# Kernel tuning notes

Measured on AMD Instinct MI355X. Metric: run time of the kernel, lower is better.

The kernel has to match this reference:

```python
import jax, jax.numpy as jnp
import numpy as np

B, T, C, H = 2, 4096, 512, 8
D = C // H          # head_size = 64
FF = 4 * C          # 2048
EPS = 1e-5


def _layernorm(x, g, b):
    mu = jnp.mean(x, axis=-1, keepdims=True)
    var = jnp.mean(jnp.square(x - mu), axis=-1, keepdims=True)
    return (x - mu) * jax.lax.rsqrt(var + EPS) * g + b


def setup_inputs() -> dict:
    key = jax.random.key(0)
    ks = jax.random.split(key, 10)
    s = 0.02
    return {
        "x":  jax.random.normal(ks[0], (B, T, C), dtype=jnp.float32),
        # per-head K/Q/V linears (bias=False) packed as [C, C] = concat over heads
        "Wq": jax.random.normal(ks[1], (C, C), dtype=jnp.float32) * s,
        "Wk": jax.random.normal(ks[2], (C, C), dtype=jnp.float32) * s,
        "Wv": jax.random.normal(ks[3], (C, C), dtype=jnp.float32) * s,
        "Wo": jax.random.normal(ks[4], (C, C), dtype=jnp.float32) * s,
        "bo": jnp.zeros((C,), dtype=jnp.float32),
        "W1": jax.random.normal(ks[5], (C, FF), dtype=jnp.float32) * s,
        "b1": jnp.zeros((FF,), dtype=jnp.float32),
        "W2": jax.random.normal(ks[6], (FF, C), dtype=jnp.float32) * s,
        "b2": jnp.zeros((C,), dtype=jnp.float32),
        "g1": jnp.ones((C,), dtype=jnp.float32),
        "be1": jnp.zeros((C,), dtype=jnp.float32),
        "g2": jnp.ones((C,), dtype=jnp.float32),
        "be2": jnp.zeros((C,), dtype=jnp.float32),
    }


def reference(x, Wq, Wk, Wv, Wo, bo, W1, b1, W2, b2, g1, be1, g2, be2):
    # --- self-attention on ln1(x), residual add ---
    h = _layernorm(x, g1, be1)                              # [B,T,C]
    q = (h @ Wq).reshape(B, T, H, D)
    k = (h @ Wk).reshape(B, T, H, D)
    v = (h @ Wv).reshape(B, T, H, D)
    # NOTE: original scales by C**-0.5 (n_embd), NOT head_size**-0.5
    scores = jnp.einsum("bthd,bshd->bhts", q, k) * (C ** -0.5)  # [B,H,T,T]
    causal = jnp.tril(jnp.ones((T, T), dtype=bool))
    scores = jnp.where(causal, scores, -jnp.inf)
    wei = jax.nn.softmax(scores, axis=-1)                   # dropout = identity (eval)
    attn = jnp.einsum("bhts,bshd->bthd", wei, v).reshape(B, T, C)
    x = x + (attn @ Wo + bo)                                # proj dropout = identity
    # --- feed-forward on ln2(x), residual add ---
    h2 = _layernorm(x, g2, be2)
    ff = jax.nn.relu(h2 @ W1 + b1) @ W2 + b2                # dropout = identity
    return x + ff
```

## Files before the change

kernel.cpp:

```cpp
#include <hip/hip_runtime.h>

typedef __attribute__((ext_vector_type(8))) __bf16 bf16x8;
typedef __attribute__((ext_vector_type(4))) __bf16 bf16x4;
typedef __attribute__((ext_vector_type(4))) float f32x4;
typedef __attribute__((ext_vector_type(4))) unsigned int u32x4;
typedef __attribute__((ext_vector_type(4))) unsigned short u16x4;
typedef __attribute__((ext_vector_type(8))) unsigned short u16x8;
typedef __attribute__((ext_vector_type(4))) short s16x4;
typedef unsigned short u16;

static __device__ __forceinline__ u16 f2b(float f) {
    unsigned u = __builtin_bit_cast(unsigned, f);
    u = (u + 0x7FFFu + ((u >> 16) & 1u)) >> 16;
    return (u16)u;
}
static __device__ __forceinline__ float b2f(u16 u) {
    return __builtin_bit_cast(float, ((unsigned)u) << 16);
}
static __device__ __forceinline__ float fexp2(float x) {
#if __has_builtin(__builtin_amdgcn_exp2f)
    return __builtin_amdgcn_exp2f(x);
#else
    return exp2f(x);
#endif
}
static __device__ __forceinline__ f32x4 mfma16(bf16x4 a, bf16x4 b, f32x4 c) {
#if __has_builtin(__builtin_amdgcn_mfma_f32_16x16x16_bf16)
    return __builtin_amdgcn_mfma_f32_16x16x16_bf16(a, b, c, 0, 0, 0);
#else
    return __builtin_amdgcn_mfma_f32_16x16x16bf16_1k(
        __builtin_bit_cast(s16x4, a), __builtin_bit_cast(s16x4, b), c, 0, 0, 0);
#endif
}

static __device__ __forceinline__ void gload16(const u16* g, u16* l) {
    __builtin_amdgcn_global_load_lds(
        (const __attribute__((address_space(1))) unsigned int*)g,
        (__attribute__((address_space(3))) unsigned int*)l, 16, 0, 0);
}

__global__ __launch_bounds__(256) void prep_w(
    const float* __restrict__ Wq, const float* __restrict__ Wk,
    const float* __restrict__ Wv, const float* __restrict__ Wo,
    const float* __restrict__ W1, const float* __restrict__ W2,
    u16* __restrict__ WqkvT, u16* __restrict__ WoT,
    u16* __restrict__ W1T, u16* __restrict__ W2T)
{
    const int z = blockIdx.z;
    const float* src; u16* dst; int K, N;
    if (z == 0)      { src = Wq; dst = WqkvT;             K = 512;  N = 512;  }
    else if (z == 1) { src = Wk; dst = WqkvT + 512*512;   K = 512;  N = 512;  }
    else if (z == 2) { src = Wv; dst = WqkvT + 1024*512;  K = 512;  N = 512;  }
    else if (z == 3) { src = Wo; dst = WoT;               K = 512;  N = 512;  }
    else if (z == 4) { src = W1; dst = W1T;               K = 512;  N = 2048; }
    else             { src = W2; dst = W2T;               K = 2048; N = 512;  }
    const int nt = blockIdx.x * 32, kt = blockIdx.y * 32;
    if (nt >= N || kt >= K) return;
    __shared__ float tile[32][33];
    const int tx = threadIdx.x & 31, ty = threadIdx.x >> 5;
    #pragma unroll
    for (int i = 0; i < 4; ++i)
        tile[ty + i*8][tx] = src[(size_t)(kt + ty + i*8) * N + nt + tx];
    __syncthreads();
    #pragma unroll
    for (int i = 0; i < 4; ++i)
        dst[(size_t)(nt + ty + i*8) * K + kt + tx] = f2b(tile[tx][ty + i*8]);
}

__global__ __launch_bounds__(256) void ln_rows(
    const float* __restrict__ x, const float* __restrict__ g,
    const float* __restrict__ b, u16* __restrict__ out)
{
    const int row = blockIdx.x * 4 + (threadIdx.x >> 6);
    const int lane = threadIdx.x & 63;
    const float* xr = x + (size_t)row * 512;
    f32x4 v0 = *(const f32x4*)(xr + lane * 4);
    f32x4 v1 = *(const f32x4*)(xr + 256 + lane * 4);
    float s = v0[0]+v0[1]+v0[2]+v0[3]+v1[0]+v1[1]+v1[2]+v1[3];
    #pragma unroll
    for (int o = 1; o < 64; o <<= 1) s += __shfl_xor(s, o);
    const float mu = s * (1.0f / 512.0f);
    float s2 = 0.f;
    #pragma unroll
    for (int i = 0; i < 4; ++i) { float d0 = v0[i]-mu, d1 = v1[i]-mu; s2 += d0*d0 + d1*d1; }
    #pragma unroll
    for (int o = 1; o < 64; o <<= 1) s2 += __shfl_xor(s2, o);
    const float inv = rsqrtf(s2 * (1.0f/512.0f) + 1e-5f);
    f32x4 g0 = *(const f32x4*)(g + lane*4), g1 = *(const f32x4*)(g + 256 + lane*4);
    f32x4 b0 = *(const f32x4*)(b + lane*4), b1 = *(const f32x4*)(b + 256 + lane*4);
    u16x4 p0, p1;
    #pragma unroll
    for (int i = 0; i < 4; ++i) {
        p0[i] = f2b((v0[i]-mu)*inv*g0[i] + b0[i]);
        p1[i] = f2b((v1[i]-mu)*inv*g1[i] + b1[i]);
    }
    u16* orow = out + (size_t)row * 512;
    *(u16x4*)(orow + lane*4)       = p0;
    *(u16x4*)(orow + 256 + lane*4) = p1;
}

template<int FLAGS>
__global__ __launch_bounds__(256) void gemm_bt(
    const u16* __restrict__ A, const u16* __restrict__ BT,
    const int N, const int K,
    const float* __restrict__ bias, const float* __restrict__ res,
    void* __restrict__ outv, u16* __restrict__ vt)
{
    __shared__ __attribute__((aligned(16))) u16 As[3][4096];
    __shared__ __attribute__((aligned(16))) u16 Bs[3][4096];
    const int tid = threadIdx.x, lane = tid & 63, w = tid >> 6;
    const int wr2 = w >> 1, wc = w & 1;
    const int m0 = blockIdx.y << 7, n0 = blockIdx.x << 7;
    const int g = lane >> 4, c = lane & 15;
    const f32x4 fz = {0.f, 0.f, 0.f, 0.f};

    f32x4 acc[4][4];
    #pragma unroll
    for (int m = 0; m < 4; ++m)
      #pragma unroll
      for (int n = 0; n < 4; ++n) acc[m][n] = fz;

    const int srow = tid >> 2;
    const int scs = (((tid & 3) ^ (srow & 3)) * 8);
    const u16* Ag = A  + (size_t)(m0 + srow)*K + scs;
    const u16* Bg = BT + (size_t)(n0 + srow)*K + scs;
    const size_t rstep = (size_t)64 * K;

    const int nkt = K >> 5;
    auto stage = [&](int slot, int kt) {
        const int k0 = kt << 5;
        u16* ad = &As[0][0] + slot*4096 + w*512;
        u16* bd = &Bs[0][0] + slot*4096 + w*512;
        gload16(Ag + k0,         ad); gload16(Ag + rstep + k0, ad + 2048);
        gload16(Bg + k0,         bd); gload16(Bg + rstep + k0, bd + 2048);
    };
    stage(0, 0);
    stage(1, (1 < nkt) ? 1 : 0);

    int rd = 0, wrs = 2;
    for (int kt = 0; kt < nkt; ++kt) {
        asm volatile("s_waitcnt vmcnt(4)" ::: "memory");
        __builtin_amdgcn_s_barrier();
        asm volatile("" ::: "memory");
        stage(wrs, (kt + 2 < nkt) ? (kt + 2) : (nkt - 1));
        const u16* Ab = &As[0][0] + rd*4096;
        const u16* Bb = &Bs[0][0] + rd*4096;
        bf16x8 af[4], bfr[4];
        #pragma unroll
        for (int m = 0; m < 4; ++m) {
            const int row = wr2*64 + m*16 + c;
            af[m] = *(const bf16x8*)(Ab + row*32 + (((g*16) ^ ((row&3)<<4)) >> 1));
        }
        #pragma unroll
        for (int n = 0; n < 4; ++n) {
            const int row = wc*64 + n*16 + c;
            bfr[n] = *(const bf16x8*)(Bb + row*32 + (((g*16) ^ ((row&3)<<4)) >> 1));
        }
        #pragma unroll
        for (int m = 0; m < 4; ++m)
          #pragma unroll
          for (int n = 0; n < 4; ++n)
            acc[m][n] = __builtin_amdgcn_mfma_f32_16x16x32_bf16(af[m], bfr[n], acc[m][n], 0, 0, 0);
        rd = (rd == 2) ? 0 : rd + 1;
        wrs = (wrs == 2) ? 0 : wrs + 1;
    }

    #pragma unroll
    for (int m = 0; m < 4; ++m) {
        const int row = m0 + wr2*64 + m*16 + 4*g;
        #pragma unroll
        for (int n = 0; n < 4; ++n) {
            const int col = n0 + wc*64 + n*16 + c;
            const float bv = (FLAGS & 1) ? bias[col] : 0.0f;
            float vv[4];
            #pragma unroll
            for (int r = 0; r < 4; ++r) {
                float v = acc[m][n][r] + bv;
                if (FLAGS & 16) v *= (col < 512) ? 0.0637587246f : 1.0f;
                if (FLAGS & 2) v += res[(size_t)(row + r)*N + col];
                if (FLAGS & 4) v = fmaxf(v, 0.0f);
                vv[r] = v;
            }
            if ((FLAGS & 32) && col >= 1024) {
                u16x4 pv;
                #pragma unroll
                for (int r = 0; r < 4; ++r) pv[r] = f2b(vv[r]);
                *(u16x4*)(vt + (size_t)((row >> 12)*512 + (col - 1024))*4096
                             + (row & 4095)) = pv;
            } else if (FLAGS & 8) {
                #pragma unroll
                for (int r = 0; r < 4; ++r)
                    ((float*)outv)[(size_t)(row + r)*N + col] = vv[r];
            } else {
                #pragma unroll
                for (int r = 0; r < 4; ++r)
                    ((u16*)outv)[(size_t)(row + r)*N + col] = f2b(vv[r]);
            }
        }
    }
}

__global__ __launch_bounds__(256, 3) void attn_fwd(
    const u16* __restrict__ qkv, const u16* __restrict__ vT,
    u16* __restrict__ part, u16* __restrict__ att)
{
    const int bh = blockIdx.y, b = bh >> 3, h = bh & 7;
    const int i = blockIdx.x;
    int qt, t0, t1, single;
    if (i < 32) { qt = i; t0 = 0; t1 = qt + 1; single = 1; }
    else {
        const int j = i - 32; qt = 32 + (j >> 1);
        const int nt = qt + 1, tm = nt >> 1;
        t0 = (j & 1) ? tm : 0; t1 = (j & 1) ? nt : tm; single = 0;
    }

    const int tid = threadIdx.x, lane = tid & 63, w = tid >> 6;
    const int g = lane >> 4, c16 = lane & 15;
    __shared__ __attribute__((aligned(16))) u16 smem[24576 + 512];
    u16* Wb = smem + w*6144;
    float* lbuf = (float*)(smem + 24576);

    const u16* qp  = qkv + (size_t)b*4096*1536 + h*64;
    const u16* kp  = qp + 512;
    const u16* vtp = vT + (size_t)bh*64*4096;

    const u16* kgA = kp + (size_t)(16*w + (lane>>3))*1536
                        + (((lane&7) ^ ((lane>>3)&7)) * 8);
    const u16* kgB = kgA + (size_t)8*1536;
    const int sd = lane >> 1;
    const u16* vgA = vtp + (size_t)sd*4096 + 16*w + (((lane&1) ^ ((sd>>2)&1)) * 8);
    const u16* vgB = vgA + (size_t)32*4096;

    const int kOff0 = c16*64 + ((g ^ (c16&7)) * 8);
    const int kOff1 = c16*64 + (((4+g) ^ (c16&7)) * 8);
    const int vroff = c16*16 + (((g>>1) ^ ((c16>>2)&1)) * 8) + (g&1)*4;

    const int Q0 = qt*64;
    bf16x8 qB[4][2];
    #pragma unroll
    for (int sub = 0; sub < 4; ++sub) {
        const u16* qr = qp + (size_t)(Q0 + sub*16 + c16)*1536 + g*8;
        qB[sub][0] = *(const bf16x8*)(qr);
        qB[sub][1] = *(const bf16x8*)(qr + 32);
    }

    const f32x4 fz = {0.f,0.f,0.f,0.f};
    f32x4 oacc[4][4];
    #pragma unroll
    for (int dt = 0; dt < 4; ++dt)
      #pragma unroll
      for (int sub = 0; sub < 4; ++sub) oacc[dt][sub] = fz;
    float lsum[4] = {0.f, 0.f, 0.f, 0.f};

    {
        const int tp1 = (t0+1 < t1) ? (t0+1) : (t1-1);
        u16* s0 = Wb + (t0 % 3)*2048;
        const size_t ko0 = (size_t)(t0 << 6)*1536; const int kv0 = t0 << 6;
        gload16(kgA + ko0, s0);        gload16(kgB + ko0, s0 + 512);
        gload16(vgA + kv0, s0 + 1024); gload16(vgB + kv0, s0 + 1536);
        u16* s1 = Wb + (tp1 % 3)*2048;
        const size_t ko1 = (size_t)(tp1 << 6)*1536; const int kv1 = tp1 << 6;
        gload16(kgA + ko1, s1);        gload16(kgB + ko1, s1 + 512);
        gload16(vgA + kv1, s1 + 1024); gload16(vgB + kv1, s1 + 1536);
    }
    int rd = t0 % 3;
    int wrs = rd + 2; if (wrs >= 3) wrs -= 3;

    for (int t = t0; t < t1; ++t) {
        asm volatile("s_waitcnt vmcnt(4)" ::: "memory");
        const u16* slotR = Wb + rd*2048;
        const bf16x8 kc0 = *(const bf16x8*)(slotR + kOff0);
        const bf16x8 kc1 = *(const bf16x8*)(slotR + kOff1);
        bf16x4 va[4];
        #pragma unroll
        for (int dt = 0; dt < 4; ++dt)
            va[dt] = *(const bf16x4*)(slotR + 1024 + dt*256 + vroff);
        {
            const int tp = (t+2 < t1) ? (t+2) : (t1-1);
            u16* slotW = Wb + wrs*2048;
            const size_t ko = (size_t)(tp << 6)*1536; const int kv = tp << 6;
            gload16(kgA + ko, slotW);        gload16(kgB + ko, slotW + 512);
            gload16(vgA + kv, slotW + 1024); gload16(vgB + kv, slotW + 1536);
        }
        f32x4 s[4];
        #pragma unroll
        for (int sub = 0; sub < 4; ++sub) {
            f32x4 sv = __builtin_amdgcn_mfma_f32_16x16x32_bf16(kc0, qB[sub][0], fz, 0, 0, 0);
            s[sub]   = __builtin_amdgcn_mfma_f32_16x16x32_bf16(kc1, qB[sub][1], sv, 0, 0, 0);
        }
        bf16x4 pt[4];
        if (t < qt) {
            #pragma unroll
            for (int sub = 0; sub < 4; ++sub) {
                float p0 = fexp2(s[sub][0]), p1 = fexp2(s[sub][1]);
                float p2 = fexp2(s[sub][2]), p3 = fexp2(s[sub][3]);
                lsum[sub] += (p0 + p1) + (p2 + p3);
                bf16x4 pv;
                pv[0] = (__bf16)p0; pv[1] = (__bf16)p1;
                pv[2] = (__bf16)p2; pv[3] = (__bf16)p3;
                pt[sub] = pv;
            }
        } else {
            const int kvbase = t*64 + 16*w + 4*g;
            #pragma unroll
            for (int sub = 0; sub < 4; ++sub) {
                const int qi = Q0 + sub*16 + c16;
                bf16x4 pv; float a = 0.f;
                #pragma unroll
                for (int r = 0; r < 4; ++r) {
                    float p = (kvbase + r <= qi) ? fexp2(s[sub][r]) : 0.0f;
                    a += p; pv[r] = (__bf16)p;
                }
                lsum[sub] += a; pt[sub] = pv;
            }
        }
        #pragma unroll
        for (int dt = 0; dt < 4; ++dt)
          #pragma unroll
          for (int sub = 0; sub < 4; ++sub)
            oacc[dt][sub] = mfma16(va[dt], pt[sub], oacc[dt][sub]);
        rd  = (rd  == 2) ? 0 : rd  + 1;
        wrs = (wrs == 2) ? 0 : wrs + 1;
    }

    #pragma unroll
    for (int sub = 0; sub < 4; ++sub) {
        float v = lsum[sub];
        v += __shfl_xor(v, 16);
        v += __shfl_xor(v, 32);
        if (g == 0) lbuf[w*64 + sub*16 + c16] = v;
    }
    __syncthreads();
    float ltot[4];
    #pragma unroll
    for (int sub = 0; sub < 4; ++sub) {
        const int qr = sub*16 + c16;
        ltot[sub] = lbuf[qr] + lbuf[64 + qr] + lbuf[128 + qr] + lbuf[192 + qr];
    }

    float* img = (float*)smem;
    f32x4 ofin[4];
    const int roff = (g ^ (c16 & 3))*4;
    #pragma unroll
    for (int dt = 0; dt < 4; ++dt) {
        #pragma unroll
        for (int sub = 0; sub < 4; ++sub)
            *(f32x4*)(img + w*1024 + (sub*16 + c16)*16 + roff) = oacc[dt][sub];
        __syncthreads();
        if (w == dt) {
            #pragma unroll
            for (int sub = 0; sub < 4; ++sub) {
                const int off = (sub*16 + c16)*16 + roff;
                f32x4 a0 = *(const f32x4*)(img + off);
                f32x4 a1 = *(const f32x4*)(img + 1024 + off);
                f32x4 a2 = *(const f32x4*)(img + 2048 + off);
                f32x4 a3 = *(const f32x4*)(img + 3072 + off);
                ofin[sub] = (a0 + a1) + (a2 + a3);
            }
        }
        __syncthreads();
    }

    const int dbase = 16*w + 4*g;
    if (single) {
        #pragma unroll
        for (int sub = 0; sub < 4; ++sub) {
            const int qrow = sub*16 + c16;
            const float inv = 1.0f / ltot[sub];
            const f32x4 o = ofin[sub];
            u16x4 ov;
            ov[0] = f2b(o[0]*inv); ov[1] = f2b(o[1]*inv);
            ov[2] = f2b(o[2]*inv); ov[3] = f2b(o[3]*inv);
            *(u16x4*)(att + (size_t)(b*4096 + Q0 + qrow)*512 + h*64 + dbase) = ov;
        }
    } else {
        u16* onum = part + (size_t)(bh*64 + (i - 32)) * 4224;
        float* lout = (float*)(onum + 4096);
        #pragma unroll
        for (int sub = 0; sub < 4; ++sub) {
            const int qrow = sub*16 + c16;
            const f32x4 o = ofin[sub];
            u16x4 ov;
            ov[0] = f2b(o[0]); ov[1] = f2b(o[1]);
            ov[2] = f2b(o[2]); ov[3] = f2b(o[3]);
            *(u16x4*)(onum + qrow*64 + dbase) = ov;
            if (w == 0 && g == 0) lout[qrow] = ltot[sub];
        }
    }
}

__global__ __launch_bounds__(256) void attn_merge(
    const u16* __restrict__ part, u16* __restrict__ att)
{
    const int qt = 32 + blockIdx.x, bh = blockIdx.y, b = bh >> 3, h = bh & 7;
    const int t = threadIdx.x;
    const int row = t >> 2, c0 = (t & 3) * 16;
    const u16* p0 = part + (size_t)(bh*64 + 2*blockIdx.x) * 4224;
    const u16* p1 = p0 + 4224;
    const float lt = ((const float*)(p0 + 4096))[row] + ((const float*)(p1 + 4096))[row];
    const float inv = 1.0f / lt;
    u16x8 a0 = *(const u16x8*)(p0 + row*64 + c0);
    u16x8 a1 = *(const u16x8*)(p0 + row*64 + c0 + 8);
    u16x8 b0q = *(const u16x8*)(p1 + row*64 + c0);
    u16x8 b1q = *(const u16x8*)(p1 + row*64 + c0 + 8);
    u16x8 o1, o2;
    #pragma unroll
    for (int j = 0; j < 8; ++j) {
        o1[j] = f2b((b2f(a0[j]) + b2f(b0q[j])) * inv);
        o2[j] = f2b((b2f(a1[j]) + b2f(b1q[j])) * inv);
    }
    u16* dst = att + (size_t)(b*4096 + qt*64 + row)*512 + h*64 + c0;
    *(u16x8*)dst = o1;
    *(u16x8*)(dst + 8) = o2;
}

extern "C" void kernel_launch(void* const* d_in, const int* in_sizes, int n_in,
                              void* d_out, int out_size, void* d_ws, size_t ws_size,
                              hipStream_t stream)
{
    (void)in_sizes; (void)n_in; (void)out_size; (void)ws_size;
    const float* x   = (const float*)d_in[0];
    const float* Wq  = (const float*)d_in[1];
    const float* Wk  = (const float*)d_in[2];
    const float* Wv  = (const float*)d_in[3];
    const float* Wo  = (const float*)d_in[4];
    const float* bo  = (const float*)d_in[5];
    const float* W1  = (const float*)d_in[6];
    const float* b1  = (const float*)d_in[7];
    const float* W2  = (const float*)d_in[8];
    const float* b2  = (const float*)d_in[9];
    const float* g1  = (const float*)d_in[10];
    const float* be1 = (const float*)d_in[11];
    const float* g2  = (const float*)d_in[12];
    const float* be2 = (const float*)d_in[13];

    char* ws = (char*)d_ws;
    u16*   WqkvT = (u16*)(ws + 0);
    u16*   WoT   = (u16*)(ws + 1572864);
    u16*   W1T   = (u16*)(ws + 2097152);
    u16*   W2T   = (u16*)(ws + 4194304);
    u16*   H     = (u16*)(ws + 6291456);
    u16*   PART  = (u16*)(ws + 6291456);
    float* X2    = (float*)(ws + 14680064);
    u16*   QKV   = (u16*)(ws + 31457280);
    u16*   VT    = (u16*)(ws + 56623104);
    u16*   ATT   = (u16*)(ws + 65011712);
    u16*   F1    = (u16*)(ws + 31457280);

    prep_w<<<dim3(64, 64, 6), 256, 0, stream>>>(Wq, Wk, Wv, Wo, W1, W2,
                                                WqkvT, WoT, W1T, W2T);
    ln_rows<<<2048, 256, 0, stream>>>(x, g1, be1, H);
    gemm_bt<48><<<dim3(12, 64), 256, 0, stream>>>(H, WqkvT, 1536, 512,
                                                  nullptr, nullptr, QKV, VT);
    attn_fwd<<<dim3(96, 16), 256, 0, stream>>>(QKV, VT, PART, ATT);
    attn_merge<<<dim3(32, 16), 256, 0, stream>>>(PART, ATT);
    gemm_bt<11><<<dim3(4, 64), 256, 0, stream>>>(ATT, WoT, 512, 512,
                                                 bo, x, X2, nullptr);
    ln_rows<<<2048, 256, 0, stream>>>(X2, g2, be2, H);
    gemm_bt<5><<<dim3(16, 64), 256, 0, stream>>>(H, W1T, 2048, 512,
                                                 b1, nullptr, F1, nullptr);
    gemm_bt<11><<<dim3(4, 64), 256, 0, stream>>>(F1, W2T, 512, 2048,
                                                 b2, X2, (float*)d_out, nullptr);
}
```

Baseline: 219.2 us.

## Use 128x64 GEMM tiles with 4-deep ring for N=512 GEMMs, compact prep grid

The N=512 GEMMs (out-projection and FFN down-projection) switch from 128x128 to 128x64 output tiles with a 4-slot LDS ring, which doubles their block count so more CUs are busy. The weight-prep launch becomes a dense 1D grid so blocks no longer exit early on out-of-range tiles. The attention loop now issues its next prefetch before waiting on the current slot, allowing deeper overlap of loads. Each GEMM block reuses its A data less, and the higher vmcnt threshold changes how outstanding loads are tracked.

After: 215.3 us. No clear change (-1.8%).

```diff
diff --git a/kernel.cpp b/kernel.cpp
--- a/kernel.cpp
+++ b/kernel.cpp
@@ -46,25 +46,33 @@
     u16* __restrict__ WqkvT, u16* __restrict__ WoT,
     u16* __restrict__ W1T, u16* __restrict__ W2T)
 {
-    const int z = blockIdx.z;
-    const float* src; u16* dst; int K, N;
-    if (z == 0)      { src = Wq; dst = WqkvT;             K = 512;  N = 512;  }
-    else if (z == 1) { src = Wk; dst = WqkvT + 512*512;   K = 512;  N = 512;  }
-    else if (z == 2) { src = Wv; dst = WqkvT + 1024*512;  K = 512;  N = 512;  }
-    else if (z == 3) { src = Wo; dst = WoT;               K = 512;  N = 512;  }
-    else if (z == 4) { src = W1; dst = W1T;               K = 512;  N = 2048; }
-    else             { src = W2; dst = W2T;               K = 2048; N = 512;  }
-    const int nt = blockIdx.x * 32, kt = blockIdx.y * 32;
-    if (nt >= N || kt >= K) return;
+    const int i = blockIdx.x;
+    const float* src; u16* dst; int K, N, nt, kt;
+    if (i < 1024) {
+        const int z = i >> 8, idx = i & 255;
+        K = 512; N = 512; nt = (idx & 15) * 32; kt = (idx >> 4) * 32;
+        if (z == 0)      { src = Wq; dst = WqkvT; }
+        else if (z == 1) { src = Wk; dst = WqkvT + 512*512; }
+        else if (z == 2) { src = Wv; dst = WqkvT + 1024*512; }
+        else             { src = Wo; dst = WoT; }
+    } else if (i < 2048) {
+        const int idx = i - 1024;
+        src = W1; dst = W1T; K = 512; N = 2048;
+        nt = (idx & 63) * 32; kt = (idx >> 6) * 32;
+    } else {
+        const int idx = i - 2048;
+        src = W2; dst = W2T; K = 2048; N = 512;
+        nt = (idx & 15) * 32; kt = (idx >> 4) * 32;
+    }
     __shared__ float tile[32][33];
     const int tx = threadIdx.x & 31, ty = threadIdx.x >> 5;
     #pragma unroll
-    for (int i = 0; i < 4; ++i)
-        tile[ty + i*8][tx] = src[(size_t)(kt + ty + i*8) * N + nt + tx];
+    for (int r = 0; r < 4; ++r)
+        tile[ty + r*8][tx] = src[(size_t)(kt + ty + r*8) * N + nt + tx];
     __syncthreads();
     #pragma unroll
-    for (int i = 0; i < 4; ++i)
-        dst[(size_t)(nt + ty + i*8) * K + kt + tx] = f2b(tile[tx][ty + i*8]);
+    for (int r = 0; r < 4; ++r)
+        dst[(size_t)(nt + ty + r*8) * K + kt + tx] = f2b(tile[tx][ty + r*8]);
 }
 
 __global__ __launch_bounds__(256) void ln_rows(
@@ -99,26 +107,27 @@
     *(u16x4*)(orow + 256 + lane*4) = p1;
 }
 
-template<int FLAGS>
+template<int FLAGS, int NB>
 __global__ __launch_bounds__(256) void gemm_bt(
     const u16* __restrict__ A, const u16* __restrict__ BT,
     const int N, const int K,
     const float* __restrict__ bias, const float* __restrict__ res,
     void* __restrict__ outv, u16* __restrict__ vt)
 {
-    __shared__ __attribute__((aligned(16))) u16 As[3][4096];
-    __shared__ __attribute__((aligned(16))) u16 Bs[3][4096];
+    constexpr int RING = (NB == 2) ? 3 : 4;
+    __shared__ __attribute__((aligned(16))) u16 As[RING * 4096];
+    __shared__ __attribute__((aligned(16))) u16 Bs[RING * 2048 * NB];
     const int tid = threadIdx.x, lane = tid & 63, w = tid >> 6;
     const int wr2 = w >> 1, wc = w & 1;
-    const int m0 = blockIdx.y << 7, n0 = blockIdx.x << 7;
+    const int m0 = blockIdx.y << 7, n0 = blockIdx.x * (64 * NB);
     const int g = lane >> 4, c = lane & 15;
     const f32x4 fz = {0.f, 0.f, 0.f, 0.f};
 
-    f32x4 acc[4][4];
+    f32x4 acc[4][2 * NB];
     #pragma unroll
     for (int m = 0; m < 4; ++m)
       #pragma unroll
-      for (int n = 0; n < 4; ++n) acc[m][n] = fz;
+      for (int n = 0; n < 2 * NB; ++n) acc[m][n] = fz;
 
     const int srow = tid >> 2;
     const int scs = (((tid & 3) ^ (srow & 3)) * 8);
@@ -129,48 +138,54 @@
     const int nkt = K >> 5;
     auto stage = [&](int slot, int kt) {
         const int k0 = kt << 5;
-        u16* ad = &As[0][0] + slot*4096 + w*512;
-        u16* bd = &Bs[0][0] + slot*4096 + w*512;
-        gload16(Ag + k0,         ad); gload16(Ag + rstep + k0, ad + 2048);
-        gload16(Bg + k0,         bd); gload16(Bg + rstep + k0, bd + 2048);
+        u16* ad = &As[0] + slot*4096 + w*512;
+        gload16(Ag + k0,         ad);
+        gload16(Ag + rstep + k0, ad + 2048);
+        u16* bd = &Bs[0] + slot*2048*NB + w*512;
+        gload16(Bg + k0, bd);
+        if constexpr (NB == 2) gload16(Bg + rstep + k0, bd + 2048);
     };
     stage(0, 0);
     stage(1, (1 < nkt) ? 1 : 0);
-
-    int rd = 0, wrs = 2;
+    if constexpr (RING == 4) stage(2, (2 < nkt) ? 2 : 0);
+
     for (int kt = 0; kt < nkt; ++kt) {
-        asm volatile("s_waitcnt vmcnt(4)" ::: "memory");
+        if constexpr (NB == 2) asm volatile("s_waitcnt vmcnt(4)" ::: "memory");
+        else                   asm volatile("s_waitcnt vmcnt(6)" ::: "memory");
         __builtin_amdgcn_s_barrier();
         asm volatile("" ::: "memory");
-        stage(wrs, (kt + 2 < nkt) ? (kt + 2) : (nkt - 1));
-        const u16* Ab = &As[0][0] + rd*4096;
-        const u16* Bb = &Bs[0][0] + rd*4096;
-        bf16x8 af[4], bfr[4];
+        {
+            int tp = kt + RING - 1; if (tp >= nkt) tp = nkt - 1;
+            int sl = kt + RING - 1; sl -= (sl / RING) * RING;
+            stage(sl, tp);
+        }
+        const int rd = kt - (kt / RING) * RING;
+        const u16* Ab = &As[0] + rd*4096;
+        const u16* Bb = &Bs[0] + rd*2048*NB;
+        bf16x8 af[4], bfr[2 * NB];
         #pragma unroll
         for (int m = 0; m < 4; ++m) {
             const int row = wr2*64 + m*16 + c;
             af[m] = *(const bf16x8*)(Ab + row*32 + (((g*16) ^ ((row&3)<<4)) >> 1));
         }
         #pragma unroll
-        for (int n = 0; n < 4; ++n) {
-            const int row = wc*64 + n*16 + c;
+        for (int n = 0; n < 2 * NB; ++n) {
+            const int row = wc*(32*NB) + n*16 + c;
             bfr[n] = *(const bf16x8*)(Bb + row*32 + (((g*16) ^ ((row&3)<<4)) >> 1));
         }
         #pragma unroll
         for (int m = 0; m < 4; ++m)
           #pragma unroll
-          for (int n = 0; n < 4; ++n)
+          for (int n = 0; n < 2 * NB; ++n)
             acc[m][n] = __builtin_amdgcn_mfma_f32_16x16x32_bf16(af[m], bfr[n], acc[m][n], 0, 0, 0);
-        rd = (rd == 2) ? 0 : rd + 1;
-        wrs = (wrs == 2) ? 0 : wrs + 1;
     }
 
     #pragma unroll
     for (int m = 0; m < 4; ++m) {
         const int row = m0 + wr2*64 + m*16 + 4*g;
         #pragma unroll
-        for (int n = 0; n < 4; ++n) {
-            const int col = n0 + wc*64 + n*16 + c;
+        for (int n = 0; n < 2 * NB; ++n) {
+            const int col = n0 + wc*(32*NB) + n*16 + c;
             const float bv = (FLAGS & 1) ? bias[col] : 0.0f;
             float vv[4];
             #pragma unroll
@@ -267,14 +282,6 @@
     int wrs = rd + 2; if (wrs >= 3) wrs -= 3;
 
     for (int t = t0; t < t1; ++t) {
-        asm volatile("s_waitcnt vmcnt(4)" ::: "memory");
-        const u16* slotR = Wb + rd*2048;
-        const bf16x8 kc0 = *(const bf16x8*)(slotR + kOff0);
-        const bf16x8 kc1 = *(const bf16x8*)(slotR + kOff1);
-        bf16x4 va[4];
-        #pragma unroll
-        for (int dt = 0; dt < 4; ++dt)
-            va[dt] = *(const bf16x4*)(slotR + 1024 + dt*256 + vroff);
         {
             const int tp = (t+2 < t1) ? (t+2) : (t1-1);
             u16* slotW = Wb + wrs*2048;
@@ -282,6 +289,14 @@
             gload16(kgA + ko, slotW);        gload16(kgB + ko, slotW + 512);
             gload16(vgA + kv, slotW + 1024); gload16(vgB + kv, slotW + 1536);
         }
+        asm volatile("s_waitcnt vmcnt(8)" ::: "memory");
+        const u16* slotR = Wb + rd*2048;
+        const bf16x8 kc0 = *(const bf16x8*)(slotR + kOff0);
+        const bf16x8 kc1 = *(const bf16x8*)(slotR + kOff1);
+        bf16x4 va[4];
+        #pragma unroll
+        for (int dt = 0; dt < 4; ++dt)
+            va[dt] = *(const bf16x4*)(slotR + 1024 + dt*256 + vroff);
         f32x4 s[4];
         #pragma unroll
         for (int sub = 0; sub < 4; ++sub) {
@@ -447,18 +462,18 @@
     u16*   ATT   = (u16*)(ws + 65011712);
     u16*   F1    = (u16*)(ws + 31457280);
 
-    prep_w<<<dim3(64, 64, 6), 256, 0, stream>>>(Wq, Wk, Wv, Wo, W1, W2,
-                                                WqkvT, WoT, W1T, W2T);
+    prep_w<<<3072, 256, 0, stream>>>(Wq, Wk, Wv, Wo, W1, W2,
+                                     WqkvT, WoT, W1T, W2T);
     ln_rows<<<2048, 256, 0, stream>>>(x, g1, be1, H);
-    gemm_bt<48><<<dim3(12, 64), 256, 0, stream>>>(H, WqkvT, 1536, 512,
-                                                  nullptr, nullptr, QKV, VT);
+    gemm_bt<48, 2><<<dim3(12, 64), 256, 0, stream>>>(H, WqkvT, 1536, 512,
+                                                     nullptr, nullptr, QKV, VT);
     attn_fwd<<<dim3(96, 16), 256, 0, stream>>>(QKV, VT, PART, ATT);
     attn_merge<<<dim3(32, 16), 256, 0, stream>>>(PART, ATT);
-    gemm_bt<11><<<dim3(4, 64), 256, 0, stream>>>(ATT, WoT, 512, 512,
-                                                 bo, x, X2, nullptr);
+    gemm_bt<11, 1><<<dim3(8, 64), 256, 0, stream>>>(ATT, WoT, 512, 512,
+                                                    bo, x, X2, nullptr);
     ln_rows<<<2048, 256, 0, stream>>>(X2, g2, be2, H);
-    gemm_bt<5><<<dim3(16, 64), 256, 0, stream>>>(H, W1T, 2048, 512,
-                                                 b1, nullptr, F1, nullptr);
-    gemm_bt<11><<<dim3(4, 64), 256, 0, stream>>>(F1, W2T, 512, 2048,
-                                                 b2, X2, (float*)d_out, nullptr);
-}
+    gemm_bt<5, 2><<<dim3(16, 64), 256, 0, stream>>>(H, W1T, 2048, 512,
+                                                    b1, nullptr, F1, nullptr);
+    gemm_bt<11, 1><<<dim3(8, 64), 256, 0, stream>>>(F1, W2T, 512, 2048,
+                                                    b2, X2, (float*)d_out, nullptr);
+}
```
